# Kernel tuning notes

Hardware: AMD Instinct MI355X
Metric: run time of the kernel (lower is better)

## Reference

```python
import jax, jax.numpy as jnp
import numpy as np

NEG_SLOPE = 0.2
BN_EPS = 1e-5


def gat_conv(x, src, dst, num_nodes, W, att_src, att_dst, bias, concat):
    # x: [N, F_in]; W: [F_in, H*C]; att_src/att_dst: [H, C]
    H, C = att_src.shape
    h = (x @ W).reshape(num_nodes, H, C)                 # [N, H, C]
    a_src = jnp.einsum('nhc,hc->nh', h, att_src)          # [N, H]
    a_dst = jnp.einsum('nhc,hc->nh', h, att_dst)          # [N, H]
    e = a_src[src] + a_dst[dst]                           # [E, H]
    e = jax.nn.leaky_relu(e, NEG_SLOPE)
    # segment softmax over edges sharing the same destination node
    m = jax.ops.segment_max(e, dst, num_segments=num_nodes)   # [N, H]
    ex = jnp.exp(e - m[dst])
    denom = jax.ops.segment_sum(ex, dst, num_segments=num_nodes)  # [N, H]
    alpha = ex / (denom[dst] + 1e-16)                     # [E, H]
    msg = h[src] * alpha[:, :, None]                      # [E, H, C]
    out = jax.ops.segment_sum(msg, dst, num_segments=num_nodes)   # [N, H, C]
    if concat:
        return out.reshape(num_nodes, H * C) + bias
    return out.mean(axis=1) + bias


def batch_norm(x, gamma, beta):
    mu = x.mean(axis=0)
    var = x.var(axis=0)
    return (x - mu) * jax.lax.rsqrt(var + BN_EPS) * gamma + beta


def setup_inputs() -> dict:
    key = jax.random.key(0)
    ks = jax.random.split(key, 16)
    N, E, F_in, C, H, NC = 50000, 800000, 128, 16, 8, 2
    s = lambda k, shape, fan: jax.random.normal(k, shape, jnp.float32) * (1.0 / np.sqrt(fan))
    inp = {
        'x': jax.random.normal(ks[0], (N, F_in), jnp.float32),
        'edge_index': jax.random.randint(ks[1], (2, E), 0, N, jnp.int32),
        'W0': s(ks[2], (F_in, H * C), F_in),
        'att_src0': s(ks[3], (H, C), C),
        'att_dst0': s(ks[4], (H, C), C),
        'b0': jnp.zeros((H * C,), jnp.float32),
        'gamma0': jnp.ones((H * C,), jnp.float32),
        'beta0': jnp.zeros((H * C,), jnp.float32),
        'W1': s(ks[5], (H * C, H * C), H * C),
        'att_src1': s(ks[6], (H, C), C),
        'att_dst1': s(ks[7], (H, C), C),
        'b1': jnp.zeros((C,), jnp.float32),
        'gamma1': jnp.ones((C,), jnp.float32),
        'beta1': jnp.zeros((C,), jnp.float32),
        'Wc': s(ks[8], (C, NC), C),
        'bc': jnp.zeros((NC,), jnp.float32),
    }
    return inp


def reference(x, edge_index, W0, att_src0, att_dst0, b0, gamma0, beta0,
              W1, att_src1, att_dst1, b1, gamma1, beta1, Wc, bc):
    N = x.shape[0]
    loop = jnp.arange(N, dtype=edge_index.dtype)
    src = jnp.concatenate([edge_index[0], loop])  # add self-loops (PyG default)
    dst = jnp.concatenate([edge_index[1], loop])
    # layer 0: concat heads -> [N, H*C]
    h = gat_conv(x, src, dst, N, W0, att_src0, att_dst0, b0, concat=True)
    h = batch_norm(h, gamma0, beta0)
    h = jax.nn.elu(h)
    # layer 1: average heads -> [N, C]
    h = gat_conv(h, src, dst, N, W1, att_src1, att_dst1, b1, concat=False)
    h = batch_norm(h, gamma1, beta1)
    logits = h @ Wc + bc
    return logits
```

## Files before the change

kernel.cpp:

```cpp
#include <hip/hip_runtime.h>
#include <math.h>

#define NEG_SLOPE 0.2f
#define BN_EPS 1e-5f


__device__ __forceinline__ void edge_sd(const int* __restrict__ ei, int E, int eid, int& s, int& d) {
    if (eid < E) { s = ei[eid]; d = ei[E + eid]; }
    else         { s = d = eid - E; }
}

__device__ __forceinline__ float lrelu(float v) { return v > 0.f ? v : NEG_SLOPE * v; }

__device__ __forceinline__ unsigned short f2bf(float f) {
    unsigned u = __float_as_uint(f);
    u += 0x7fffu + ((u >> 16) & 1u);
    return (unsigned short)(u >> 16);
}

__global__ __launch_bounds__(256) void gemm128(const float* __restrict__ X,
                                               const float* __restrict__ W,
                                               float* __restrict__ Y,
                                               unsigned short* __restrict__ Ybf,
                                               const float* __restrict__ bnmu,
                                               const float* __restrict__ bnrs,
                                               const float* __restrict__ gamma,
                                               const float* __restrict__ beta,
                                               int Nrows) {
    __shared__ float xs[64 * 128];
    int bm = blockIdx.x * 64;
    int tid = threadIdx.x;

    const float4* Xv = (const float4*)(X + (size_t)bm * 128);
    float4* xsv = (float4*)xs;
    if (bnmu == nullptr) {
        for (int i = tid; i < 64 * 32; i += 256) {
            int row = i >> 5;
            xsv[i] = (bm + row < Nrows) ? Xv[i] : make_float4(0.f, 0.f, 0.f, 0.f);
        }
    } else {
        for (int i = tid; i < 64 * 32; i += 256) {
            int row = i >> 5;
            int cb = (i & 31) * 4;
            float4 v = (bm + row < Nrows) ? Xv[i] : make_float4(0.f, 0.f, 0.f, 0.f);
            float4 m4 = *(const float4*)(bnmu + cb);
            float4 r4 = *(const float4*)(bnrs + cb);
            float4 g4 = *(const float4*)(gamma + cb);
            float4 b4 = *(const float4*)(beta + cb);
            v.x = (v.x - m4.x) * r4.x * g4.x + b4.x;
            v.y = (v.y - m4.y) * r4.y * g4.y + b4.y;
            v.z = (v.z - m4.z) * r4.z * g4.z + b4.z;
            v.w = (v.w - m4.w) * r4.w * g4.w + b4.w;
            v.x = v.x > 0.f ? v.x : expm1f(v.x);
            v.y = v.y > 0.f ? v.y : expm1f(v.y);
            v.z = v.z > 0.f ? v.z : expm1f(v.z);
            v.w = v.w > 0.f ? v.w : expm1f(v.w);
            xsv[i] = v;
        }
    }
    __syncthreads();

    int cq = tid & 31;
    int rg = tid >> 5;

    float acc[8][4];
#pragma unroll
    for (int r = 0; r < 8; r++)
#pragma unroll
        for (int j = 0; j < 4; j++) acc[r][j] = 0.f;

    const float* xbase = xs + (rg * 8) * 128;
#pragma unroll 4
    for (int k = 0; k < 128; k++) {
        float4 w4 = *(const float4*)(W + k * 128 + cq * 4);
#pragma unroll
        for (int r = 0; r < 8; r++) {
            float xv = xbase[r * 128 + k];
            acc[r][0] += xv * w4.x;
            acc[r][1] += xv * w4.y;
            acc[r][2] += xv * w4.z;
            acc[r][3] += xv * w4.w;
        }
    }
#pragma unroll
    for (int r = 0; r < 8; r++) {
        int row = bm + rg * 8 + r;
        if (row < Nrows) {
            *(float4*)(Y + (size_t)row * 128 + cq * 4) =
                make_float4(acc[r][0], acc[r][1], acc[r][2], acc[r][3]);
            ushort4 pk;
            pk.x = f2bf(acc[r][0]);
            pk.y = f2bf(acc[r][1]);
            pk.z = f2bf(acc[r][2]);
            pk.w = f2bf(acc[r][3]);
            *(ushort4*)(Ybf + (size_t)row * 128 + cq * 4) = pk;
        }
    }
}

__global__ void att_kernel(const float* __restrict__ Hm,
                           const float* __restrict__ att_s,
                           const float* __restrict__ att_d,
                           float* __restrict__ a_src, float* __restrict__ a_dst, int N) {
    int idx = blockIdx.x * 256 + threadIdx.x;
    if (idx >= N * 8) return;
    int n = idx >> 3, h = idx & 7;
    const float* hp = Hm + (size_t)n * 128 + h * 16;
    float ss = 0.f, sd = 0.f;
#pragma unroll
    for (int c = 0; c < 16; c++) {
        float v = hp[c];
        ss += v * att_s[h * 16 + c];
        sd += v * att_d[h * 16 + c];
    }
    a_src[idx] = ss;
    a_dst[idx] = sd;
}

__global__ void hist_kernel(const int* __restrict__ ei, int E, int Etot,
                            int* __restrict__ counts, int* __restrict__ rank) {
    int eid = blockIdx.x * 256 + threadIdx.x;
    if (eid >= Etot) return;
    int s, d;
    edge_sd(ei, E, eid, s, d);
    rank[eid] = atomicAdd(&counts[d], 1);
}

__global__ __launch_bounds__(256) void chunksum_kernel(const int* __restrict__ counts,
                                                       int* __restrict__ csum, int N) {
    __shared__ int red[256];
    int base = blockIdx.x * 1024;
    int s = 0;
    for (int i = threadIdx.x; i < 1024; i += 256) {
        int idx = base + i;
        s += (idx < N) ? counts[idx] : 0;
    }
    red[threadIdx.x] = s;
    __syncthreads();
#pragma unroll
    for (int st = 128; st > 0; st >>= 1) {
        if (threadIdx.x < st) red[threadIdx.x] += red[threadIdx.x + st];
        __syncthreads();
    }
    if (threadIdx.x == 0) csum[blockIdx.x] = red[0];
}

__global__ void chunkscan_kernel(int* __restrict__ csum, int nchunk) {
    int lane = threadIdx.x;
    int v = (lane < nchunk) ? csum[lane] : 0;
    int incl = v;
#pragma unroll
    for (int off = 1; off < 64; off <<= 1) {
        int t = __shfl_up(incl, off);
        if (lane >= off) incl += t;
    }
    if (lane < nchunk) csum[lane] = incl - v;
}

__global__ __launch_bounds__(1024) void scanfinal_kernel(const int* __restrict__ counts,
                                                         const int* __restrict__ csum,
                                                         int* __restrict__ rowptr, int N) {
    __shared__ int wsum[16], woff_s[16];
    int tid = threadIdx.x, lane = tid & 63, wid = tid >> 6;
    int idx = blockIdx.x * 1024 + tid;
    int v = (idx < N) ? counts[idx] : 0;
    int incl = v;
#pragma unroll
    for (int off = 1; off < 64; off <<= 1) {
        int t = __shfl_up(incl, off);
        if (lane >= off) incl += t;
    }
    if (lane == 63) wsum[wid] = incl;
    __syncthreads();
    if (wid == 0 && lane < 16) {
        int w = wsum[lane], iw = w;
#pragma unroll
        for (int off = 1; off < 16; off <<= 1) {
            int t = __shfl_up(iw, off);
            if (lane >= off) iw += t;
        }
        woff_s[lane] = iw - w;
    }
    __syncthreads();
    if (idx < N) rowptr[idx + 1] = csum[blockIdx.x] + woff_s[wid] + incl;
    if (blockIdx.x == 0 && tid == 0) rowptr[0] = 0;
}

__global__ void scatter_kernel(const int* __restrict__ ei, int E, int Etot,
                               const int* __restrict__ rowptr, const int* __restrict__ rank,
                               unsigned short* __restrict__ ssrc) {
    int eid = blockIdx.x * 256 + threadIdx.x;
    if (eid >= Etot) return;
    int s, d;
    edge_sd(ei, E, eid, s, d);
    ssrc[rowptr[d] + rank[eid]] = (unsigned short)s;
}

template <bool MEAN>
__global__ __launch_bounds__(256) void agg_kernel(const int* __restrict__ rowptr,
                                                  const unsigned short* __restrict__ ssrc,
                                                  const float* __restrict__ a_src,
                                                  const float* __restrict__ a_dst,
                                                  const unsigned short* __restrict__ Hbf,
                                                  float* __restrict__ outbuf, int N) {
    int wid = threadIdx.x >> 6;
    int dst = blockIdx.x * 4 + wid;
    if (dst >= N) return;
    int lane = threadIdx.x & 63;
    int j  = lane >> 3;
    int hj = lane & 7;
    int hf = lane >> 3;
    int f  = lane * 2;
    int start = rowptr[dst], end = rowptr[dst + 1];
    float adst = a_dst[dst * 8 + hj];

    float acc0 = 0.f, acc1 = 0.f, denl = 0.f;
    for (int base = start; base < end; base += 8) {
        int i = base + j;
        int s = (i < end) ? (int)ssrc[i] : -1;
        float w = 0.f;
        if (s >= 0) w = __expf(lrelu(a_src[s * 8 + hj] + adst));
        denl += w;

        int   sA[8];
        float wA[8];
        unsigned uA[8];
#pragma unroll
        for (int j2 = 0; j2 < 8; j2++) {
            sA[j2] = __shfl(s, j2 * 8);
            wA[j2] = __shfl(w, j2 * 8 + hf);
        }
#pragma unroll
        for (int j2 = 0; j2 < 8; j2++)
            uA[j2] = (sA[j2] >= 0) ? *(const unsigned*)(Hbf + (size_t)sA[j2] * 128 + f) : 0u;
#pragma unroll
        for (int j2 = 0; j2 < 8; j2++) {
            acc0 += wA[j2] * __uint_as_float(uA[j2] << 16);
            acc1 += wA[j2] * __uint_as_float(uA[j2] & 0xffff0000u);
        }
    }
#pragma unroll
    for (int off = 8; off < 64; off <<= 1) denl += __shfl_xor(denl, off);
    float den = __shfl(denl, hf);
    float inv = 1.f / (den + 1e-16f);
    if (!MEAN) {
        *(float2*)(outbuf + (size_t)dst * 128 + f) = make_float2(acc0 * inv, acc1 * inv);
    } else {
        float r0 = acc0 * inv, r1 = acc1 * inv;
#pragma unroll
        for (int off = 8; off < 64; off <<= 1) {
            r0 += __shfl_xor(r0, off);
            r1 += __shfl_xor(r1, off);
        }
        if (lane < 8)
            *(float2*)(outbuf + (size_t)dst * 16 + lane * 2) =
                make_float2(r0 * 0.125f, r1 * 0.125f);
    }
}

template <int C>
__global__ __launch_bounds__(256) void stats_part_kernel(const float* __restrict__ X, int Nrows,
                                                         float* __restrict__ partial,
                                                         int rows_per_block) {
    constexpr int GSZ = 256 / C;
    __shared__ float ls[256], lq[256];
    int c = threadIdx.x % C;
    int g = threadIdx.x / C;
    long base = (long)blockIdx.x * rows_per_block;
    long endr = base + rows_per_block;
    if (endr > Nrows) endr = Nrows;
    float s = 0.f, q = 0.f;
    for (long r = base + g; r < endr; r += GSZ) {
        float v = X[r * C + c];
        s += v;
        q += v * v;
    }
    ls[threadIdx.x] = s;
    lq[threadIdx.x] = q;
    __syncthreads();
#pragma unroll
    for (int st = GSZ / 2; st > 0; st >>= 1) {
        if (g < st) {
            ls[threadIdx.x] += ls[threadIdx.x + st * C];
            lq[threadIdx.x] += lq[threadIdx.x + st * C];
        }
        __syncthreads();
    }
    if (g == 0) {
        partial[(size_t)blockIdx.x * (2 * C) + c] = ls[c];
        partial[(size_t)blockIdx.x * (2 * C) + C + c] = lq[c];
    }
}

template <int C>
__global__ __launch_bounds__(1024) void stats_final_kernel(const float* __restrict__ partial,
                                                           int nblk, float invN,
                                                           float* __restrict__ mu,
                                                           float* __restrict__ rsig) {
    constexpr int G = 1024 / C;
    __shared__ float ls[1024], lq[1024];
    int c = threadIdx.x % C;
    int g = threadIdx.x / C;
    float s = 0.f, q = 0.f;
    for (int b = g; b < nblk; b += G) {
        s += partial[(size_t)b * (2 * C) + c];
        q += partial[(size_t)b * (2 * C) + C + c];
    }
    ls[threadIdx.x] = s;
    lq[threadIdx.x] = q;
    __syncthreads();
#pragma unroll
    for (int st = G / 2; st > 0; st >>= 1) {
        if (g < st) {
            ls[threadIdx.x] += ls[threadIdx.x + st * C];
            lq[threadIdx.x] += lq[threadIdx.x + st * C];
        }
        __syncthreads();
    }
    if (g == 0) {
        float m_ = ls[c] * invN;
        float v = lq[c] * invN - m_ * m_;
        mu[c] = m_;
        rsig[c] = rsqrtf(v + BN_EPS);
    }
}

__global__ void final_kernel(const float* __restrict__ out1,
                             const float* __restrict__ mu, const float* __restrict__ rsig,
                             const float* __restrict__ gamma, const float* __restrict__ beta,
                             const float* __restrict__ Wc, const float* __restrict__ bc,
                             float* __restrict__ out, int N) {
    int n = blockIdx.x * 256 + threadIdx.x;
    if (n >= N) return;
    float l0 = bc[0], l1 = bc[1];
#pragma unroll
    for (int c = 0; c < 16; c++) {
        float v = (out1[(size_t)n * 16 + c] - mu[c]) * rsig[c] * gamma[c] + beta[c];
        l0 += v * Wc[c * 2 + 0];
        l1 += v * Wc[c * 2 + 1];
    }
    out[(size_t)n * 2 + 0] = l0;
    out[(size_t)n * 2 + 1] = l1;
}

extern "C" void kernel_launch(void* const* d_in, const int* in_sizes, int n_in,
                              void* d_out, int out_size, void* d_ws, size_t ws_size,
                              hipStream_t stream) {
    const float* x   = (const float*)d_in[0];
    const int*   ei  = (const int*)d_in[1];
    const float* W0  = (const float*)d_in[2];
    const float* as0 = (const float*)d_in[3];
    const float* ad0 = (const float*)d_in[4];
    const float* g0  = (const float*)d_in[6];
    const float* be0 = (const float*)d_in[7];
    const float* W1  = (const float*)d_in[8];
    const float* as1 = (const float*)d_in[9];
    const float* ad1 = (const float*)d_in[10];
    const float* g1  = (const float*)d_in[12];
    const float* be1 = (const float*)d_in[13];
    const float* Wc  = (const float*)d_in[14];
    const float* bc  = (const float*)d_in[15];
    float* out = (float*)d_out;

    int N = in_sizes[0] / 128;
    int E = in_sizes[1] / 2;
    int Etot = E + N;

    char* ws = (char*)d_ws;
    size_t off = 0;
    auto walloc = [&](size_t bytes) -> void* {
        void* p = ws + off;
        off += (bytes + 255) & ~(size_t)255;
        return p;
    };
    float*          A       = (float*)walloc((size_t)N * 128 * 4);
    float*          B       = (float*)walloc((size_t)N * 128 * 4);
    unsigned short* Hbf     = (unsigned short*)walloc((size_t)N * 128 * 2);
    float*          a_src   = (float*)walloc((size_t)N * 8 * 4);
    float*          a_dst   = (float*)walloc((size_t)N * 8 * 4);
    float*          out1    = (float*)walloc((size_t)N * 16 * 4);
    int*            counts  = (int*)walloc((size_t)N * 4);
    int*            rowptr  = (int*)walloc((size_t)(N + 1) * 4);
    int*            rank    = (int*)walloc((size_t)Etot * 4);
    int*            csum    = (int*)walloc(64 * 4);
    unsigned short* ssrc    = (unsigned short*)walloc((size_t)Etot * 2);
    float*          partial = (float*)walloc((size_t)256 * 256 * 4);
    float*          stats   = (float*)walloc(2 * 128 * 4);
    float* mu = stats, * rsig = stats + 128;

    dim3 b256(256);
    int gN64    = (N + 63) / 64;
    int gNH     = (N * 8 + 255) / 256;
    int gE      = (Etot + 255) / 256;
    int gAgg    = (N + 3) / 4;
    int nchunk  = (N + 1023) / 1024;
    const int SBLK = 256;
    int rpb = (N + SBLK - 1) / SBLK;

    hipMemsetAsync(counts, 0, (size_t)N * 4, stream);
    hist_kernel<<<gE, b256, 0, stream>>>(ei, E, Etot, counts, rank);
    chunksum_kernel<<<nchunk, b256, 0, stream>>>(counts, csum, N);
    chunkscan_kernel<<<1, 64, 0, stream>>>(csum, nchunk);
    scanfinal_kernel<<<nchunk, 1024, 0, stream>>>(counts, csum, rowptr, N);
    scatter_kernel<<<gE, b256, 0, stream>>>(ei, E, Etot, rowptr, rank, ssrc);

    gemm128<<<gN64, b256, 0, stream>>>(x, W0, A, Hbf, nullptr, nullptr, nullptr, nullptr, N);
    att_kernel<<<gNH, b256, 0, stream>>>(A, as0, ad0, a_src, a_dst, N);
    agg_kernel<false><<<gAgg, b256, 0, stream>>>(rowptr, ssrc, a_src, a_dst, Hbf, B, N);
    stats_part_kernel<128><<<SBLK, b256, 0, stream>>>(B, N, partial, rpb);
    stats_final_kernel<128><<<1, 1024, 0, stream>>>(partial, SBLK, 1.0f / N, mu, rsig);

    gemm128<<<gN64, b256, 0, stream>>>(B, W1, B, Hbf, mu, rsig, g0, be0, N);
    att_kernel<<<gNH, b256, 0, stream>>>(B, as1, ad1, a_src, a_dst, N);
    agg_kernel<true><<<gAgg, b256, 0, stream>>>(rowptr, ssrc, a_src, a_dst, Hbf, out1, N);
    stats_part_kernel<16><<<SBLK, b256, 0, stream>>>(out1, N, partial, rpb);
    stats_final_kernel<16><<<1, 1024, 0, stream>>>(partial, SBLK, 1.0f / N, mu, rsig);
    final_kernel<<<(N + 255) / 256, b256, 0, stream>>>(out1, mu, rsig, g1, be1, Wc, bc, out, N);
}
```

Before: 357.7 us.

## Use bf16 MFMA for node GEMMs and fuse attention-score computation

Replaces the fp32 scalar FMA GEMM with a bf16 MFMA 16x16x32 kernel that reads a pre-transposed bf16 weight matrix. The attention logits a_src/a_dst are now computed in the GEMM epilogue with wave shuffles, which removes the separate att_kernel and the fp32 H write and re-read. Inputs and weights are rounded to bf16 before the multiply, so the attention logits lose precision compared with the fp32 path. A small transpose kernel is added to convert both weight matrices.

```diff
diff --git a/kernel.cpp b/kernel.cpp
--- a/kernel.cpp
+++ b/kernel.cpp
@@ -3,6 +3,10 @@
 
 #define NEG_SLOPE 0.2f
 #define BN_EPS 1e-5f
+
+typedef __attribute__((ext_vector_type(8))) short bf16x8;
+typedef __attribute__((ext_vector_type(4))) float f32x4;
+typedef __attribute__((ext_vector_type(8))) unsigned short us8;
 
 
 __device__ __forceinline__ void edge_sd(const int* __restrict__ ei, int E, int eid, int& s, int& d) {
@@ -18,103 +22,104 @@
     return (unsigned short)(u >> 16);
 }
 
-__global__ __launch_bounds__(256) void gemm128(const float* __restrict__ X,
-                                               const float* __restrict__ W,
-                                               float* __restrict__ Y,
-                                               unsigned short* __restrict__ Ybf,
-                                               const float* __restrict__ bnmu,
-                                               const float* __restrict__ bnrs,
-                                               const float* __restrict__ gamma,
-                                               const float* __restrict__ beta,
-                                               int Nrows) {
-    __shared__ float xs[64 * 128];
+__global__ void wtrans_kernel(const float* __restrict__ W0, const float* __restrict__ W1,
+                              unsigned short* __restrict__ Wt0, unsigned short* __restrict__ Wt1) {
+    int idx = blockIdx.x * 256 + threadIdx.x;
+    const float* W = (idx < 16384) ? W0 : W1;
+    unsigned short* Wt = (idx < 16384) ? Wt0 : Wt1;
+    int i = idx & 16383;
+    int k = i >> 7, n = i & 127;
+    Wt[n * 128 + k] = f2bf(W[k * 128 + n]);
+}
+
+__global__ __launch_bounds__(256) void gemm_att_kernel(const float* __restrict__ X,
+                                                       const unsigned short* __restrict__ Wt,
+                                                       unsigned short* __restrict__ Hbf,
+                                                       float* __restrict__ a_src,
+                                                       float* __restrict__ a_dst,
+                                                       const float* __restrict__ att_s,
+                                                       const float* __restrict__ att_d,
+                                                       const float* __restrict__ bnmu,
+                                                       const float* __restrict__ bnrs,
+                                                       const float* __restrict__ gamma,
+                                                       const float* __restrict__ beta,
+                                                       int Nrows) {
+    __shared__ unsigned short xs[64 * 136];
     int bm = blockIdx.x * 64;
     int tid = threadIdx.x;
 
-    const float4* Xv = (const float4*)(X + (size_t)bm * 128);
-    float4* xsv = (float4*)xs;
-    if (bnmu == nullptr) {
-        for (int i = tid; i < 64 * 32; i += 256) {
-            int row = i >> 5;
-            xsv[i] = (bm + row < Nrows) ? Xv[i] : make_float4(0.f, 0.f, 0.f, 0.f);
-        }
-    } else {
-        for (int i = tid; i < 64 * 32; i += 256) {
-            int row = i >> 5;
-            int cb = (i & 31) * 4;
-            float4 v = (bm + row < Nrows) ? Xv[i] : make_float4(0.f, 0.f, 0.f, 0.f);
-            float4 m4 = *(const float4*)(bnmu + cb);
-            float4 r4 = *(const float4*)(bnrs + cb);
-            float4 g4 = *(const float4*)(gamma + cb);
-            float4 b4 = *(const float4*)(beta + cb);
-            v.x = (v.x - m4.x) * r4.x * g4.x + b4.x;
-            v.y = (v.y - m4.y) * r4.y * g4.y + b4.y;
-            v.z = (v.z - m4.z) * r4.z * g4.z + b4.z;
-            v.w = (v.w - m4.w) * r4.w * g4.w + b4.w;
-            v.x = v.x > 0.f ? v.x : expm1f(v.x);
-            v.y = v.y > 0.f ? v.y : expm1f(v.y);
-            v.z = v.z > 0.f ? v.z : expm1f(v.z);
-            v.w = v.w > 0.f ? v.w : expm1f(v.w);
-            xsv[i] = v;
-        }
-    }
-    __syncthreads();
-
-    int cq = tid & 31;
-    int rg = tid >> 5;
-
-    float acc[8][4];
-#pragma unroll
-    for (int r = 0; r < 8; r++)
-#pragma unroll
-        for (int j = 0; j < 4; j++) acc[r][j] = 0.f;
-
-    const float* xbase = xs + (rg * 8) * 128;
-#pragma unroll 4
-    for (int k = 0; k < 128; k++) {
-        float4 w4 = *(const float4*)(W + k * 128 + cq * 4);
-#pragma unroll
-        for (int r = 0; r < 8; r++) {
-            float xv = xbase[r * 128 + k];
-            acc[r][0] += xv * w4.x;
-            acc[r][1] += xv * w4.y;
-            acc[r][2] += xv * w4.z;
-            acc[r][3] += xv * w4.w;
-        }
-    }
-#pragma unroll
-    for (int r = 0; r < 8; r++) {
-        int row = bm + rg * 8 + r;
-        if (row < Nrows) {
-            *(float4*)(Y + (size_t)row * 128 + cq * 4) =
-                make_float4(acc[r][0], acc[r][1], acc[r][2], acc[r][3]);
-            ushort4 pk;
-            pk.x = f2bf(acc[r][0]);
-            pk.y = f2bf(acc[r][1]);
-            pk.z = f2bf(acc[r][2]);
-            pk.w = f2bf(acc[r][3]);
-            *(ushort4*)(Ybf + (size_t)row * 128 + cq * 4) = pk;
-        }
-    }
-}
-
-__global__ void att_kernel(const float* __restrict__ Hm,
-                           const float* __restrict__ att_s,
-                           const float* __restrict__ att_d,
-                           float* __restrict__ a_src, float* __restrict__ a_dst, int N) {
-    int idx = blockIdx.x * 256 + threadIdx.x;
-    if (idx >= N * 8) return;
-    int n = idx >> 3, h = idx & 7;
-    const float* hp = Hm + (size_t)n * 128 + h * 16;
-    float ss = 0.f, sd = 0.f;
-#pragma unroll
-    for (int c = 0; c < 16; c++) {
-        float v = hp[c];
-        ss += v * att_s[h * 16 + c];
-        sd += v * att_d[h * 16 + c];
-    }
-    a_src[idx] = ss;
-    a_dst[idx] = sd;
+    for (int i = tid; i < 64 * 16; i += 256) {
+        int row = i >> 4;
+        int c8 = (i & 15) * 8;
+        int grow = bm + row;
+        float v[8];
+        if (grow < Nrows) {
+            float4 v0 = *(const float4*)(X + (size_t)grow * 128 + c8);
+            float4 v1 = *(const float4*)(X + (size_t)grow * 128 + c8 + 4);
+            v[0] = v0.x; v[1] = v0.y; v[2] = v0.z; v[3] = v0.w;
+            v[4] = v1.x; v[5] = v1.y; v[6] = v1.z; v[7] = v1.w;
+        } else {
+#pragma unroll
+            for (int j = 0; j < 8; j++) v[j] = 0.f;
+        }
+        if (bnmu != nullptr) {
+#pragma unroll
+            for (int j = 0; j < 8; j++) {
+                int c = c8 + j;
+                float t = (v[j] - bnmu[c]) * bnrs[c] * gamma[c] + beta[c];
+                v[j] = t > 0.f ? t : expm1f(t);
+            }
+        }
+        us8 p;
+#pragma unroll
+        for (int j = 0; j < 8; j++) p[j] = f2bf(v[j]);
+        *(us8*)(xs + row * 136 + c8) = p;
+    }
+    __syncthreads();
+
+    int w = tid >> 6, lane = tid & 63;
+    int m16 = lane & 15;
+    int quad = lane >> 4;
+
+    f32x4 acc[8];
+#pragma unroll
+    for (int c = 0; c < 8; c++) acc[c] = (f32x4){0.f, 0.f, 0.f, 0.f};
+
+    const unsigned short* xrow = xs + (w * 16 + m16) * 136 + quad * 8;
+#pragma unroll
+    for (int ks = 0; ks < 4; ks++) {
+        bf16x8 a = *(const bf16x8*)(xrow + ks * 32);
+#pragma unroll
+        for (int c = 0; c < 8; c++) {
+            bf16x8 b = *(const bf16x8*)(Wt + (c * 16 + m16) * 128 + ks * 32 + quad * 8);
+            acc[c] = __builtin_amdgcn_mfma_f32_16x16x32_bf16(a, b, acc[c], 0, 0, 0);
+        }
+    }
+
+#pragma unroll
+    for (int c = 0; c < 8; c++) {
+        float asw = att_s[c * 16 + m16];
+        float adw = att_d[c * 16 + m16];
+#pragma unroll
+        for (int r = 0; r < 4; r++) {
+            int row = bm + w * 16 + quad * 4 + r;
+            float hv = acc[c][r];
+            float p = hv * asw;
+            float q = hv * adw;
+#pragma unroll
+            for (int off = 1; off < 16; off <<= 1) {
+                p += __shfl_xor(p, off);
+                q += __shfl_xor(q, off);
+            }
+            if (row < Nrows) {
+                Hbf[(size_t)row * 128 + c * 16 + m16] = f2bf(hv);
+                if (m16 == 0) {
+                    a_src[row * 8 + c] = p;
+                    a_dst[row * 8 + c] = q;
+                }
+            }
+        }
+    }
 }
 
 __global__ void hist_kernel(const int* __restrict__ ei, int E, int Etot,
@@ -373,9 +378,10 @@
         off += (bytes + 255) & ~(size_t)255;
         return p;
     };
-    float*          A       = (float*)walloc((size_t)N * 128 * 4);
     float*          B       = (float*)walloc((size_t)N * 128 * 4);
     unsigned short* Hbf     = (unsigned short*)walloc((size_t)N * 128 * 2);
+    unsigned short* Wt0     = (unsigned short*)walloc(128 * 128 * 2);
+    unsigned short* Wt1     = (unsigned short*)walloc(128 * 128 * 2);
     float*          a_src   = (float*)walloc((size_t)N * 8 * 4);
     float*          a_dst   = (float*)walloc((size_t)N * 8 * 4);
     float*          out1    = (float*)walloc((size_t)N * 16 * 4);
@@ -390,7 +396,6 @@
 
     dim3 b256(256);
     int gN64    = (N + 63) / 64;
-    int gNH     = (N * 8 + 255) / 256;
     int gE      = (Etot + 255) / 256;
     int gAgg    = (N + 3) / 4;
     int nchunk  = (N + 1023) / 1024;
@@ -404,14 +409,16 @@
     scanfinal_kernel<<<nchunk, 1024, 0, stream>>>(counts, csum, rowptr, N);
     scatter_kernel<<<gE, b256, 0, stream>>>(ei, E, Etot, rowptr, rank, ssrc);
 
-    gemm128<<<gN64, b256, 0, stream>>>(x, W0, A, Hbf, nullptr, nullptr, nullptr, nullptr, N);
-    att_kernel<<<gNH, b256, 0, stream>>>(A, as0, ad0, a_src, a_dst, N);
+    wtrans_kernel<<<128, b256, 0, stream>>>(W0, W1, Wt0, Wt1);
+
+    gemm_att_kernel<<<gN64, b256, 0, stream>>>(x, Wt0, Hbf, a_src, a_dst, as0, ad0,
+                                               nullptr, nullptr, nullptr, nullptr, N);
     agg_kernel<false><<<gAgg, b256, 0, stream>>>(rowptr, ssrc, a_src, a_dst, Hbf, B, N);
     stats_part_kernel<128><<<SBLK, b256, 0, stream>>>(B, N, partial, rpb);
     stats_final_kernel<128><<<1, 1024, 0, stream>>>(partial, SBLK, 1.0f / N, mu, rsig);
 
-    gemm128<<<gN64, b256, 0, stream>>>(B, W1, B, Hbf, mu, rsig, g0, be0, N);
-    att_kernel<<<gNH, b256, 0, stream>>>(B, as1, ad1, a_src, a_dst, N);
+    gemm_att_kernel<<<gN64, b256, 0, stream>>>(B, Wt1, Hbf, a_src, a_dst, as1, ad1,
+                                               mu, rsig, g0, be0, N);
     agg_kernel<true><<<gAgg, b256, 0, stream>>>(rowptr, ssrc, a_src, a_dst, Hbf, out1, N);
     stats_part_kernel<16><<<SBLK, b256, 0, stream>>>(out1, N, partial, rpb);
     stats_final_kernel<16><<<1, 1024, 0, stream>>>(partial, SBLK, 1.0f / N, mu, rsig);
```

After: 397.9 us. +11.3%, slower.
